# Kernel tuning notes

Measured on AMD Instinct MI355X. Metric: run time of the kernel, lower is better.

## Reference

```python
import jax, jax.numpy as jnp
import numpy as np
from math import comb

N_INPUT, N_HIDDEN, N_LATENT = 2, 1024, 16
T, B = 320, 192
DEG = N_LATENT // 2 - 1          # 7
NPTS = DEG + 1                   # 8 control points
LAT = N_LATENT + N_LATENT // 2   # 24

_COMB = jnp.array([comb(DEG, i) for i in range(NPTS)], dtype=jnp.float32)
_I = jnp.arange(NPTS, dtype=jnp.float32)


def setup_inputs() -> dict:
    key = jax.random.key(0)
    ks = jax.random.split(key, 24)
    H = N_HIDDEN
    w = lambda k, shape, sc: (jax.random.normal(k, shape, jnp.float32) * sc)
    return dict(
        x=jax.random.normal(ks[0], (T, B, N_INPUT), jnp.float32),
        latent_ctrlpt=jax.random.normal(ks[1], (B, N_LATENT), jnp.float32),
        latent_ratw=jax.random.uniform(ks[2], (B, N_LATENT // 2), jnp.float32, 0.1, 1.0),
        # h0/c0 projection linears (forward/backward directions)
        W_hf=w(ks[3], (H, LAT), 0.2), b_hf=jnp.zeros((H,), jnp.float32),
        W_hb=w(ks[4], (H, LAT), 0.2), b_hb=jnp.zeros((H,), jnp.float32),
        W_cf=w(ks[5], (H, LAT), 0.2), b_cf=jnp.zeros((H,), jnp.float32),
        W_cb=w(ks[6], (H, LAT), 0.2), b_cb=jnp.zeros((H,), jnp.float32),
        # bi-LSTM weights, PyTorch gate order (i, f, g, o)
        W_ih_f=w(ks[7], (4 * H, N_INPUT), 0.03), W_hh_f=w(ks[8], (4 * H, H), 0.03),
        b_ih_f=jnp.zeros((4 * H,), jnp.float32), b_hh_f=jnp.zeros((4 * H,), jnp.float32),
        W_ih_b=w(ks[9], (4 * H, N_INPUT), 0.03), W_hh_b=w(ks[10], (4 * H, H), 0.03),
        b_ih_b=jnp.zeros((4 * H,), jnp.float32), b_hh_b=jnp.zeros((4 * H,), jnp.float32),
        # t-logits head
        W_log=w(ks[11], (1, 2 * H), 0.03), b_log=jnp.zeros((1,), jnp.float32),
    )


def _lstm_dir(x_tm, h0, c0, W_ih, W_hh, b_ih, b_hh, reverse):
    # x_tm: (T, B, in). Precompute input projection once (compute-efficient).
    xs = jnp.einsum('tbi,gi->tbg', x_tm, W_ih) + b_ih + b_hh  # (T, B, 4H)

    def step(carry, xt):
        h, c = carry
        g = xt + h @ W_hh.T
        i, f, gg, o = jnp.split(g, 4, axis=-1)
        c = jax.nn.sigmoid(f) * c + jax.nn.sigmoid(i) * jnp.tanh(gg)
        h = jax.nn.sigmoid(o) * jnp.tanh(c)
        return (h, c), h

    _, hs = jax.lax.scan(step, (h0, c0), xs, reverse=reverse)
    return hs  # (T, B, H)


def reference(x, latent_ctrlpt, latent_ratw,
              W_hf, b_hf, W_hb, b_hb, W_cf, b_cf, W_cb, b_cb,
              W_ih_f, W_hh_f, b_ih_f, b_hh_f,
              W_ih_b, W_hh_b, b_ih_b, b_hh_b,
              W_log, b_log):
    latent = jnp.concatenate([latent_ctrlpt, latent_ratw], axis=1)  # (B, LAT)
    h0f = jnp.tanh(latent @ W_hf.T + b_hf)
    h0b = jnp.tanh(latent @ W_hb.T + b_hb)
    c0f = jnp.tanh(latent @ W_cf.T + b_cf)
    c0b = jnp.tanh(latent @ W_cb.T + b_cb)

    hf = _lstm_dir(x, h0f, c0f, W_ih_f, W_hh_f, b_ih_f, b_hh_f, reverse=False)
    hb = _lstm_dir(x, h0b, c0b, W_ih_b, W_hh_b, b_ih_b, b_hh_b, reverse=True)
    out = jnp.concatenate([hf, hb], axis=-1)           # (T, B, 2H)
    out = jnp.transpose(out, (1, 0, 2))                # batch_first (B, T, 2H)

    logits = (out @ W_log.T + b_log)[..., 0]           # (B, T)
    ts = jnp.cumsum(jax.nn.softmax(logits, axis=1), axis=1)  # (B, T) in (0, 1]

    P = latent_ctrlpt.reshape(-1, NPTS, 2)             # (B, NPTS, 2)
    r = latent_ratw.reshape(-1, NPTS)                  # (B, NPTS)

    # Rational Bezier curve, batched over B and T (replaces per-sample loop)
    t = ts[..., None]                                   # (B, T, 1)
    basis = _COMB * t ** _I * (1.0 - t) ** (DEG - _I)   # (B, T, NPTS)
    num = basis * r[:, None, :]
    w = num / num.sum(-1, keepdims=True)
    curves = jnp.einsum('btn,bnd->btd', w, P)           # (B, T, 2)

    # mean of squared consecutive control-point distances, averaged over batch
    d2 = ((P[:, 1:, :] - P[:, :-1, :]) ** 2).sum(-1)    # (B, NPTS-1)
    reg = d2.mean()
    return curves, reg
```

## Files before the change

### kernel.cpp

```cpp
#include <hip/hip_runtime.h>
#include <stdint.h>

#define T_STEPS 320
#define BATCH   192
#define HID     1024
#define NBLK    256

typedef unsigned short u16;
typedef __bf16 bf16x8 __attribute__((ext_vector_type(8)));
typedef float  f32x4  __attribute__((ext_vector_type(4)));
typedef unsigned int u32x4 __attribute__((ext_vector_type(4)));

#define OFF_BAR      0u
#define OFF_PART     16384u
#define MEMSET_BYTES 3948544u
#define OFF_C0       3948544u
#define OFF_H        5521408u
#define OFF_WPACK    7094272u
#define OFF_COEF     23871488u
#define WS_NEED      24002560u
#define OFF_HT       24002560u
#define PANEL_ELEMS  196608u
#define DIR_ELEMS    (321u * PANEL_ELEMS)
#define WS_NEED_BIG  (OFF_HT + 2ull * DIR_ELEMS * 2ull)

#define DMP_OFF_B    131072
#define DMP_WK_STRIDE 1632
#define DYN_LDS      157200

__device__ __forceinline__ u16 f2bf(float f) {
  unsigned u = __float_as_uint(f);
  unsigned r = (u + 0x7FFFu + ((u >> 16) & 1u)) >> 16;
  return (u16)r;
}
__device__ __forceinline__ float sigm(float x)   { return 1.f / (1.f + __expf(-x)); }
__device__ __forceinline__ float tanh_f(float x) { return 1.f - 2.f / (1.f + __expf(2.f * x)); }

__global__ void pack_k(const float* __restrict__ Whhf, const float* __restrict__ Whhb,
                       u16* __restrict__ wpack)
{
  int lin = blockIdx.x * 256 + threadIdx.x;
  int lane = lin & 63;
  int cg   = (lin >> 6) & 3;
  int ks   = (lin >> 8) & 31;
  int jsl  = (lin >> 13) & 63;
  int dir  = (lin >> 19) & 1;
  int col  = cg * 16 + (lane & 15);
  int R    = (col & 3) * 1024 + jsl * 16 + (col >> 2);
  int kb   = ks * 32 + (lane >> 4) * 8;
  const float* W = dir ? Whhb : Whhf;
  const float* src = W + (size_t)R * 1024 + kb;
  unsigned w[4];
  #pragma unroll
  for (int e = 0; e < 4; ++e) {
    unsigned lo = f2bf(src[2 * e]);
    unsigned hi = f2bf(src[2 * e + 1]);
    w[e] = lo | (hi << 16);
  }
  *((uint4*)(wpack + (size_t)lin * 8)) = make_uint4(w[0], w[1], w[2], w[3]);
}

__global__ void coef_k(const float* __restrict__ Wihf, const float* __restrict__ bihf,
                       const float* __restrict__ bhhf,
                       const float* __restrict__ Wihb, const float* __restrict__ bihb,
                       const float* __restrict__ bhhb, float* __restrict__ coef)
{
  int id  = blockIdx.x * 256 + threadIdx.x;
  int col = id & 63;
  int jsl = (id >> 6) & 63;
  int dir = (id >> 12) & 1;
  int R   = (col & 3) * 1024 + jsl * 16 + (col >> 2);
  const float* Wih = dir ? Wihb : Wihf;
  const float* bi  = dir ? bihb : bihf;
  const float* bh  = dir ? bhhb : bhhf;
  float4 v;
  v.x = Wih[(size_t)R * 2 + 0];
  v.y = Wih[(size_t)R * 2 + 1];
  v.z = bi[R] + bh[R];
  v.w = 0.f;
  ((float4*)coef)[id] = v;
}

__global__ void init_k(const float* __restrict__ ctrl, const float* __restrict__ ratw,
                       const float* __restrict__ Whf, const float* __restrict__ bhf,
                       const float* __restrict__ Whb, const float* __restrict__ bhb,
                       const float* __restrict__ Wcf, const float* __restrict__ bcf,
                       const float* __restrict__ Wcb, const float* __restrict__ bcb,
                       u16* hb, float* c0, size_t hstride)
{
  int idx = blockIdx.x * 256 + threadIdx.x;
  int m = blockIdx.y;
  int b = idx >> 10;
  int h = idx & 1023;
  const float* W  = (m == 0) ? Whf : (m == 1) ? Whb : (m == 2) ? Wcf : Wcb;
  const float* bi = (m == 0) ? bhf : (m == 1) ? bhb : (m == 2) ? bcf : bcb;
  float acc = bi[h];
  const float* wr = W + h * 24;
  #pragma unroll
  for (int k = 0; k < 16; ++k) acc += wr[k] * ctrl[b * 16 + k];
  #pragma unroll
  for (int k = 0; k < 8; ++k)  acc += wr[16 + k] * ratw[b * 8 + k];
  acc = tanh_f(acc);
  if (m < 2) hb[(size_t)m * hstride + (size_t)b * HID + h] = f2bf(acc);
  else       c0[((size_t)(m - 2) * BATCH + b) * HID + h] = acc;
}


#define ALD_B(S, OB) \
  asm volatile("global_load_dwordx4 %0, %1, off offset:" #OB " sc0 sc1" : "=v"(aq[S][0]) : "v"(ab0)); \
  asm volatile("global_load_dwordx4 %0, %1, off offset:" #OB " sc0 sc1" : "=v"(aq[S][1]) : "v"(ab1)); \
  asm volatile("global_load_dwordx4 %0, %1, off offset:" #OB " sc0 sc1" : "=v"(aq[S][2]) : "v"(ab2));

#define ALD_C(S, OB) \
  asm volatile("global_load_dwordx4 %0, %1, off offset:" #OB : "=v"(aq[S][0]) : "v"(ab0)); \
  asm volatile("global_load_dwordx4 %0, %1, off offset:" #OB : "=v"(aq[S][1]) : "v"(ab1)); \
  asm volatile("global_load_dwordx4 %0, %1, off offset:" #OB : "=v"(aq[S][2]) : "v"(ab2));

#define BLDS(P, C) { \
  bv[P][0] = *(const bf16x8*)(bWl + (C) * 2048 + 0);   \
  bv[P][1] = *(const bf16x8*)(bWl + (C) * 2048 + 512); \
  bv[P][2] = *(const bf16x8*)(bWl + (C) * 2048 + 1024);\
  bv[P][3] = *(const bf16x8*)(bWl + (C) * 2048 + 1536); }

#define WB(n) \
  asm volatile("s_waitcnt vmcnt(" #n ")" ::: "memory"); \
  __builtin_amdgcn_sched_barrier(0);

#define MM(C, P) { \
  _Pragma("unroll") \
  for (int mt_ = 0; mt_ < 3; ++mt_) { \
    bf16x8 a_ = __builtin_bit_cast(bf16x8, aq[C][mt_]); \
    _Pragma("unroll") \
    for (int n_ = 0; n_ < 4; ++n_) { \
      acc[mt_][n_] = __builtin_amdgcn_mfma_f32_16x16x32_bf16(a_, bv[P][n_], acc[mt_][n_], 0, 0, 0); \
    } \
  } }

#define HST(PT, VL) asm volatile("global_store_short %0, %1, off sc0 sc1" :: "v"(PT), "v"(VL) : "memory")

template<int HIST>
__launch_bounds__(512, 1)
__global__ void lstm_persist(const float* __restrict__ x,
                             const float* __restrict__ wlog,
                             float* part,
                             const float* __restrict__ c0,
                             u16* hb,
                             const u16* __restrict__ wpack,
                             const float* __restrict__ coef,
                             unsigned* bar)
{
  extern __shared__ char lds[];
  u16*   Wlds = (u16*)lds;
  float* DMP  = (float*)(lds + DMP_OFF_B);
  int*   ldsflag = (int*)(lds + DMP_OFF_B + 26112);

  const int tid   = threadIdx.x;
  const int bid   = blockIdx.x;
  const int dir   = bid >> 7;
  const int bhalf = (bid >> 6) & 1;
  const int jsl   = bid & 63;
  const int wave  = tid >> 6;
  const int lane  = tid & 63;
  const int wm    = wave >> 2;
  const int wk    = wave & 3;
  const int grp   = dir * 2 + bhalf;
  const int q4    = (lane >> 4) * 4;
  const int cl    = lane & 15;

  if (tid == 0) *ldsflag = 0;

  {
    const uint4* wsrc = (const uint4*)wpack + (size_t)(dir * 64 + jsl) * 8192;
    uint4* wdst = (uint4*)Wlds;
    #pragma unroll
    for (int i = 0; i < 16; ++i) wdst[tid + i * 512] = wsrc[tid + i * 512];
  }

  const int j    = tid & 15;
  const int rloc = tid >> 4;
  const bool pw  = (tid < 384);
  const int jglob = jsl * 16 + j;
  float4 cf0, cf1, cf2, cf3;
  {
    const float4* cp = (const float4*)coef + ((dir * 64 + jsl) * 64 + j * 4);
    cf0 = cp[0]; cf1 = cp[1]; cf2 = cp[2]; cf3 = cp[3];
  }
  const float wlg = wlog[dir * 1024 + jglob];

  float creg[4];
  int   bgm[4];
  #pragma unroll
  for (int p = 0; p < 4; ++p) {
    int bg = bhalf * 96 + p * 24 + rloc;
    bgm[p]  = bg;
    creg[p] = pw ? c0[((size_t)dir * BATCH + bg) * HID + jglob] : 0.f;
  }

  const int arow0 = bhalf * 96 + wm * 48 + 0 * 16 + cl;
  const int arow1 = arow0 + 16;
  const int arow2 = arow0 + 32;
  const int koff  = wk * 256 + (lane >> 4) * 8;
  const u16* bWl  = Wlds + (size_t)wk * 16384 + lane * 8;

  float* pbase = part + ((size_t)(dir * 8 + (jsl & 7)) * BATCH) * T_STEPS;

  unsigned* gflags = bar + grp * 1024;
  unsigned* myflag = gflags + jsl * 16;
  const unsigned* pollp = gflags + lane * 16;

  float lpv[4];
  int   lpo[4];

  __syncthreads();

  for (int s = 0; s < T_STEPS; ++s) {
    const u16* hsrc;
    u16*       hdst;
    if constexpr (HIST) {
      hsrc = hb + (size_t)dir * DIR_ELEMS + (size_t)s * PANEL_ELEMS;
      hdst = hb + (size_t)dir * DIR_ELEMS + (size_t)(s + 1) * PANEL_ELEMS;
    } else {
      const int rbuf = s & 1;
      hsrc = hb + (size_t)(dir * 2 + rbuf) * BATCH * HID;
      hdst = hb + (size_t)(dir * 2 + (rbuf ^ 1)) * BATCH * HID;
    }
    const u16* ab0 = hsrc + (size_t)arow0 * HID + koff;
    const u16* ab1 = hsrc + (size_t)arow1 * HID + koff;
    const u16* ab2 = hsrc + (size_t)arow2 * HID + koff;

    f32x4 acc[3][4];
    #pragma unroll
    for (int mt = 0; mt < 3; ++mt)
      #pragma unroll
      for (int n = 0; n < 4; ++n)
        acc[mt][n] = (f32x4){0.f, 0.f, 0.f, 0.f};

    u32x4  aq[8][3];
    bf16x8 bv[2][4];

    if constexpr (HIST) {
      ALD_C(0, 0)   ALD_C(1, 64)  ALD_C(2, 128) ALD_C(3, 192)
      ALD_C(4, 256) ALD_C(5, 320) ALD_C(6, 384) ALD_C(7, 448)
    } else {
      ALD_B(0, 0)   ALD_B(1, 64)  ALD_B(2, 128) ALD_B(3, 192)
      ALD_B(4, 256) ALD_B(5, 320) ALD_B(6, 384) ALD_B(7, 448)
    }

    BLDS(0, 0)
    BLDS(1, 1) WB(21) MM(0, 0)
    BLDS(0, 2) WB(18) MM(1, 1)
    BLDS(1, 3) WB(15) MM(2, 0)
    BLDS(0, 4) WB(12) MM(3, 1)
    BLDS(1, 5) WB(9)  MM(4, 0)
    BLDS(0, 6) WB(6)  MM(5, 1)
    BLDS(1, 7) WB(3)  MM(6, 0)
               WB(0)  MM(7, 1)

    const int t_x = dir ? (T_STEPS - 1 - s) : s;

    #pragma unroll
    for (int p = 0; p < 4; ++p) {
      if (wm == (p >> 1)) {
        const int plo = (p & 1) * 24;
        float* dst = DMP + wk * DMP_WK_STRIDE;
        #pragma unroll
        for (int mt = 0; mt < 3; ++mt)
          #pragma unroll
          for (int n = 0; n < 4; ++n)
            #pragma unroll
            for (int r = 0; r < 4; ++r) {
              int row = mt * 16 + q4 + r;
              if (row >= plo && row < plo + 24)
                dst[(row - plo) * 68 + n * 16 + cl] = acc[mt][n][r];
            }
      }
      __syncthreads();

      if (pw) {
        const int ga = rloc * 68 + (j >> 2) * 16 + (j & 3) * 4;
        f32x4 p0 = *(const f32x4*)(DMP + 0 * DMP_WK_STRIDE + ga);
        f32x4 p1 = *(const f32x4*)(DMP + 1 * DMP_WK_STRIDE + ga);
        f32x4 p2 = *(const f32x4*)(DMP + 2 * DMP_WK_STRIDE + ga);
        f32x4 p3 = *(const f32x4*)(DMP + 3 * DMP_WK_STRIDE + ga);
        f32x4 g4 = (p0 + p1) + (p2 + p3);
        int bg = bgm[p];
        float2 xv = *(const float2*)(x + ((size_t)t_x * BATCH + bg) * 2);
        float pi = g4[0] + cf0.x * xv.x + cf0.y * xv.y + cf0.z;
        float pf = g4[1] + cf1.x * xv.x + cf1.y * xv.y + cf1.z;
        float pg = g4[2] + cf2.x * xv.x + cf2.y * xv.y + cf2.z;
        float po = g4[3] + cf3.x * xv.x + cf3.y * xv.y + cf3.z;
        float ig = sigm(pi), fg = sigm(pf), gv = tanh_f(pg), og = sigm(po);
        float c = fg * creg[p] + ig * gv;
        creg[p] = c;
        float h = og * tanh_f(c);
        u16* hp = hdst + (size_t)bg * HID + jglob;
        unsigned hv = (unsigned)f2bf(h);
        HST(hp, hv);
        float lp = h * wlg;
        lp += __shfl_xor(lp, 1);
        lp += __shfl_xor(lp, 2);
        lp += __shfl_xor(lp, 4);
        lp += __shfl_xor(lp, 8);
        lpv[p] = lp;
        lpo[p] = bg * T_STEPS + t_x;
      }
      __syncthreads();
    }

    asm volatile("s_waitcnt vmcnt(0)" ::: "memory");
    __syncthreads();

    if (pw && j == 0) {
      atomicAdd(&pbase[lpo[0]], lpv[0]);
      atomicAdd(&pbase[lpo[1]], lpv[1]);
      atomicAdd(&pbase[lpo[2]], lpv[2]);
      atomicAdd(&pbase[lpo[3]], lpv[3]);
    }

    if (tid == 0) {
      unsigned nv = (unsigned)(s + 1);
      asm volatile("global_store_dword %0, %1, off sc0 sc1" :: "v"(myflag), "v"(nv) : "memory");
    }
    if (wave == 0) {
      const unsigned tgt = (unsigned)(s + 1);
      long guard = 0;
      for (;;) {
        unsigned fv;
        asm volatile("global_load_dword %0, %1, off sc0 sc1" : "=v"(fv) : "v"(pollp));
        asm volatile("s_waitcnt vmcnt(0)" ::: "memory");
        if (__all(fv >= tgt)) break;
        if (++guard > (1L << 20)) { if (lane == 0) *ldsflag = 1; break; }
        __builtin_amdgcn_s_sleep(1);
      }
    }
    __syncthreads();
    if (*ldsflag) return;
  }
}

__global__ void post_k(const float* __restrict__ part, const float* __restrict__ ctrl,
                       const float* __restrict__ ratw, float* __restrict__ out)
{
  __shared__ float sh[T_STEPS + 64];
  const int b = blockIdx.x;
  const int t = threadIdx.x;
  float l = 0.f;
  #pragma unroll
  for (int p = 0; p < 16; ++p)
    l += part[((size_t)p * BATCH + b) * T_STEPS + t];
  sh[t] = l;
  __syncthreads();
  if (t < 64) {
    float mm = sh[t];
    for (int i = t + 64; i < T_STEPS; i += 64) mm = fmaxf(mm, sh[i]);
    #pragma unroll
    for (int o = 32; o; o >>= 1) mm = fmaxf(mm, __shfl_xor(mm, o));
    if (t == 0) sh[T_STEPS] = mm;
  }
  __syncthreads();
  const float m = sh[T_STEPS];
  float e = __expf(l - m);
  __syncthreads();
  sh[t] = e;
  __syncthreads();
  for (int off = 1; off < T_STEPS; off <<= 1) {
    float v = (t >= off) ? sh[t - off] : 0.f;
    __syncthreads();
    sh[t] += v;
    __syncthreads();
  }
  const float total = sh[T_STEPS - 1];
  const float ts = sh[t] / total;

  float px[8], py[8], rr[8];
  #pragma unroll
  for (int n = 0; n < 8; ++n) {
    px[n] = ctrl[b * 16 + 2 * n];
    py[n] = ctrl[b * 16 + 2 * n + 1];
    rr[n] = ratw[b * 8 + n];
  }
  const float C[8] = {1.f, 7.f, 21.f, 35.f, 35.f, 21.f, 7.f, 1.f};
  float tp[8], up[8];
  tp[0] = 1.f; up[0] = 1.f;
  const float u = 1.f - ts;
  #pragma unroll
  for (int n = 1; n < 8; ++n) { tp[n] = tp[n - 1] * ts; up[n] = up[n - 1] * u; }
  float den = 0.f, nx = 0.f, ny = 0.f;
  #pragma unroll
  for (int n = 0; n < 8; ++n) {
    float w = C[n] * tp[n] * up[7 - n] * rr[n];
    den += w; nx += w * px[n]; ny += w * py[n];
  }
  out[(b * T_STEPS + t) * 2 + 0] = nx / den;
  out[(b * T_STEPS + t) * 2 + 1] = ny / den;

  if (b == 0) {
    __syncthreads();
    if (t < BATCH) {
      float s2 = 0.f;
      #pragma unroll
      for (int n = 0; n < 7; ++n) {
        float dx = ctrl[t * 16 + 2 * n + 2] - ctrl[t * 16 + 2 * n + 0];
        float dy = ctrl[t * 16 + 2 * n + 3] - ctrl[t * 16 + 2 * n + 1];
        s2 += dx * dx + dy * dy;
      }
      sh[t] = s2;
    }
    __syncthreads();
    if (t == 0) {
      float tot = 0.f;
      for (int i = 0; i < BATCH; ++i) tot += sh[i];
      out[BATCH * T_STEPS * 2] = tot / (float)(BATCH * 7);
    }
  }
}

extern "C" void kernel_launch(void* const* d_in, const int* in_sizes, int n_in,
                              void* d_out, int out_size, void* d_ws, size_t ws_size,
                              hipStream_t stream)
{
  const float* x    = (const float*)d_in[0];
  const float* ctrl = (const float*)d_in[1];
  const float* ratw = (const float*)d_in[2];
  const float* Whf  = (const float*)d_in[3];
  const float* bhf  = (const float*)d_in[4];
  const float* Whb  = (const float*)d_in[5];
  const float* bhb  = (const float*)d_in[6];
  const float* Wcf  = (const float*)d_in[7];
  const float* bcf  = (const float*)d_in[8];
  const float* Wcb  = (const float*)d_in[9];
  const float* bcb  = (const float*)d_in[10];
  const float* Wihf = (const float*)d_in[11];
  const float* Whhf = (const float*)d_in[12];
  const float* bihf = (const float*)d_in[13];
  const float* bhhf = (const float*)d_in[14];
  const float* Wihb = (const float*)d_in[15];
  const float* Whhb = (const float*)d_in[16];
  const float* bihb = (const float*)d_in[17];
  const float* bhhb = (const float*)d_in[18];
  const float* Wlog = (const float*)d_in[19];
  float* out = (float*)d_out;
  char*  ws  = (char*)d_ws;
  if (ws_size < (size_t)WS_NEED) return;

  const bool big = (ws_size >= (size_t)WS_NEED_BIG);

  unsigned* bar    = (unsigned*)(ws + OFF_BAR);
  float*    part   = (float*)(ws + OFF_PART);
  float*    c0     = (float*)(ws + OFF_C0);
  u16*      hsmall = (u16*)(ws + OFF_H);
  u16*      hbig   = (u16*)(ws + OFF_HT);
  u16*      wpack  = (u16*)(ws + OFF_WPACK);
  float*    coef   = (float*)(ws + OFF_COEF);

  u16*   hb      = big ? hbig : hsmall;
  size_t hstride = big ? (size_t)DIR_ELEMS : (size_t)2 * BATCH * HID;

  hipMemsetAsync(ws, 0, MEMSET_BYTES, stream);
  pack_k<<<4096, 256, 0, stream>>>(Whhf, Whhb, wpack);
  coef_k<<<32, 256, 0, stream>>>(Wihf, bihf, bhhf, Wihb, bihb, bhhb, coef);
  init_k<<<dim3(768, 4), 256, 0, stream>>>(ctrl, ratw, Whf, bhf, Whb, bhb,
                                           Wcf, bcf, Wcb, bcb, hb, c0, hstride);
  if (big) {
    hipFuncSetAttribute((const void*)lstm_persist<1>,
                        hipFuncAttributeMaxDynamicSharedMemorySize, DYN_LDS);
    lstm_persist<1><<<NBLK, 512, DYN_LDS, stream>>>(x, Wlog, part, c0, hb, wpack, coef, bar);
  } else {
    hipFuncSetAttribute((const void*)lstm_persist<0>,
                        hipFuncAttributeMaxDynamicSharedMemorySize, DYN_LDS);
    lstm_persist<0><<<NBLK, 512, DYN_LDS, stream>>>(x, Wlog, part, c0, hb, wpack, coef, bar);
  }
  post_k<<<BATCH, T_STEPS, 0, stream>>>(part, ctrl, ratw, out);
}
```

Baseline: 3.717 ms.

## Use ring of hidden-state panels with periodic cache invalidation

Replaces the full per-timestep hidden-state history (which needed a very large workspace) with a ring of P panels sized from the available workspace. The cached-load path, which reads h without cache bypass, now stays correct by issuing buffer_inv every P-2 steps, before any panel is reused. This lets the cached path run with smaller workspaces, at the cost of occasional invalidations and an extra block barrier. It also moves the step-completion flag store ahead of the logit atomics so other blocks are released sooner.

```diff
diff --git a/kernel.cpp b/kernel.cpp
--- a/kernel.cpp
+++ b/kernel.cpp
@@ -21,8 +21,8 @@
 #define WS_NEED      24002560u
 #define OFF_HT       24002560u
 #define PANEL_ELEMS  196608u
-#define DIR_ELEMS    (321u * PANEL_ELEMS)
-#define WS_NEED_BIG  (OFF_HT + 2ull * DIR_ELEMS * 2ull)
+#define PANEL_BYTES  393216u
+#define P_COST       786432u
 
 #define DMP_OFF_B    131072
 #define DMP_WK_STRIDE 1632
@@ -116,29 +116,29 @@
   asm volatile("global_load_dwordx4 %0, %1, off offset:" #OB : "=v"(aq[S][1]) : "v"(ab1)); \
   asm volatile("global_load_dwordx4 %0, %1, off offset:" #OB : "=v"(aq[S][2]) : "v"(ab2));
 
-#define BLDS(P, C) { \
-  bv[P][0] = *(const bf16x8*)(bWl + (C) * 2048 + 0);   \
-  bv[P][1] = *(const bf16x8*)(bWl + (C) * 2048 + 512); \
-  bv[P][2] = *(const bf16x8*)(bWl + (C) * 2048 + 1024);\
-  bv[P][3] = *(const bf16x8*)(bWl + (C) * 2048 + 1536); }
+#define BLDS(P_, C) { \
+  bv[P_][0] = *(const bf16x8*)(bWl + (C) * 2048 + 0);   \
+  bv[P_][1] = *(const bf16x8*)(bWl + (C) * 2048 + 512); \
+  bv[P_][2] = *(const bf16x8*)(bWl + (C) * 2048 + 1024);\
+  bv[P_][3] = *(const bf16x8*)(bWl + (C) * 2048 + 1536); }
 
 #define WB(n) \
   asm volatile("s_waitcnt vmcnt(" #n ")" ::: "memory"); \
   __builtin_amdgcn_sched_barrier(0);
 
-#define MM(C, P) { \
+#define MM(C, P_) { \
   _Pragma("unroll") \
   for (int mt_ = 0; mt_ < 3; ++mt_) { \
     bf16x8 a_ = __builtin_bit_cast(bf16x8, aq[C][mt_]); \
     _Pragma("unroll") \
     for (int n_ = 0; n_ < 4; ++n_) { \
-      acc[mt_][n_] = __builtin_amdgcn_mfma_f32_16x16x32_bf16(a_, bv[P][n_], acc[mt_][n_], 0, 0, 0); \
+      acc[mt_][n_] = __builtin_amdgcn_mfma_f32_16x16x32_bf16(a_, bv[P_][n_], acc[mt_][n_], 0, 0, 0); \
     } \
   } }
 
 #define HST(PT, VL) asm volatile("global_store_short %0, %1, off sc0 sc1" :: "v"(PT), "v"(VL) : "memory")
 
-template<int HIST>
+template<int CACHED>
 __launch_bounds__(512, 1)
 __global__ void lstm_persist(const float* __restrict__ x,
                              const float* __restrict__ wlog,
@@ -147,7 +147,8 @@
                              u16* hb,
                              const u16* __restrict__ wpack,
                              const float* __restrict__ coef,
-                             unsigned* bar)
+                             unsigned* bar,
+                             int PN, int IV)
 {
   extern __shared__ char lds[];
   u16*   Wlds = (u16*)lds;
@@ -211,19 +212,27 @@
   float lpv[4];
   int   lpo[4];
 
+  int sp   = 0;
+  int invc = 0;
+
   __syncthreads();
 
   for (int s = 0; s < T_STEPS; ++s) {
-    const u16* hsrc;
-    u16*       hdst;
-    if constexpr (HIST) {
-      hsrc = hb + (size_t)dir * DIR_ELEMS + (size_t)s * PANEL_ELEMS;
-      hdst = hb + (size_t)dir * DIR_ELEMS + (size_t)(s + 1) * PANEL_ELEMS;
-    } else {
-      const int rbuf = s & 1;
-      hsrc = hb + (size_t)(dir * 2 + rbuf) * BATCH * HID;
-      hdst = hb + (size_t)(dir * 2 + (rbuf ^ 1)) * BATCH * HID;
-    }
+    if constexpr (CACHED) {
+      if (invc == 0) {
+        if (wave == 0) {
+          asm volatile("buffer_inv sc0 sc1" ::: "memory");
+          asm volatile("s_waitcnt vmcnt(0)" ::: "memory");
+        }
+        __syncthreads();
+      }
+      if (++invc >= IV) invc = 0;
+    }
+
+    int dp = sp + 1; if (dp == PN) dp = 0;
+    const u16* hsrc = hb + ((size_t)(dir * PN + sp)) * PANEL_ELEMS;
+    u16*       hdst = hb + ((size_t)(dir * PN + dp)) * PANEL_ELEMS;
+    sp = dp;
     const u16* ab0 = hsrc + (size_t)arow0 * HID + koff;
     const u16* ab1 = hsrc + (size_t)arow1 * HID + koff;
     const u16* ab2 = hsrc + (size_t)arow2 * HID + koff;
@@ -238,7 +247,7 @@
     u32x4  aq[8][3];
     bf16x8 bv[2][4];
 
-    if constexpr (HIST) {
+    if constexpr (CACHED) {
       ALD_C(0, 0)   ALD_C(1, 64)  ALD_C(2, 128) ALD_C(3, 192)
       ALD_C(4, 256) ALD_C(5, 320) ALD_C(6, 384) ALD_C(7, 448)
     } else {
@@ -310,16 +319,15 @@
     asm volatile("s_waitcnt vmcnt(0)" ::: "memory");
     __syncthreads();
 
+    if (tid == 0) {
+      unsigned nv = (unsigned)(s + 1);
+      asm volatile("global_store_dword %0, %1, off sc0 sc1" :: "v"(myflag), "v"(nv) : "memory");
+    }
     if (pw && j == 0) {
       atomicAdd(&pbase[lpo[0]], lpv[0]);
       atomicAdd(&pbase[lpo[1]], lpv[1]);
       atomicAdd(&pbase[lpo[2]], lpv[2]);
       atomicAdd(&pbase[lpo[3]], lpv[3]);
-    }
-
-    if (tid == 0) {
-      unsigned nv = (unsigned)(s + 1);
-      asm volatile("global_store_dword %0, %1, off sc0 sc1" :: "v"(myflag), "v"(nv) : "memory");
     }
     if (wave == 0) {
       const unsigned tgt = (unsigned)(s + 1);
@@ -443,32 +451,37 @@
   char*  ws  = (char*)d_ws;
   if (ws_size < (size_t)WS_NEED) return;
 
-  const bool big = (ws_size >= (size_t)WS_NEED_BIG);
+  size_t availB = (ws_size > (size_t)OFF_HT) ? (ws_size - (size_t)OFF_HT) : 0;
+  long Pl = (long)(availB / (size_t)P_COST);
+  int P = (int)(Pl > 322 ? 322 : Pl);
+  const bool cached = (P >= 18);
 
   unsigned* bar    = (unsigned*)(ws + OFF_BAR);
   float*    part   = (float*)(ws + OFF_PART);
   float*    c0     = (float*)(ws + OFF_C0);
   u16*      hsmall = (u16*)(ws + OFF_H);
-  u16*      hbig   = (u16*)(ws + OFF_HT);
+  u16*      hring  = (u16*)(ws + OFF_HT);
   u16*      wpack  = (u16*)(ws + OFF_WPACK);
   float*    coef   = (float*)(ws + OFF_COEF);
 
-  u16*   hb      = big ? hbig : hsmall;
-  size_t hstride = big ? (size_t)DIR_ELEMS : (size_t)2 * BATCH * HID;
+  u16*   hb      = cached ? hring : hsmall;
+  int    PN      = cached ? P : 2;
+  int    IV      = (cached && P < 322) ? (P - 2) : (1 << 30);
+  size_t hstride = (size_t)PN * PANEL_ELEMS;
 
   hipMemsetAsync(ws, 0, MEMSET_BYTES, stream);
   pack_k<<<4096, 256, 0, stream>>>(Whhf, Whhb, wpack);
   coef_k<<<32, 256, 0, stream>>>(Wihf, bihf, bhhf, Wihb, bihb, bhhb, coef);
   init_k<<<dim3(768, 4), 256, 0, stream>>>(ctrl, ratw, Whf, bhf, Whb, bhb,
                                            Wcf, bcf, Wcb, bcb, hb, c0, hstride);
-  if (big) {
+  if (cached) {
     hipFuncSetAttribute((const void*)lstm_persist<1>,
                         hipFuncAttributeMaxDynamicSharedMemorySize, DYN_LDS);
-    lstm_persist<1><<<NBLK, 512, DYN_LDS, stream>>>(x, Wlog, part, c0, hb, wpack, coef, bar);
+    lstm_persist<1><<<NBLK, 512, DYN_LDS, stream>>>(x, Wlog, part, c0, hb, wpack, coef, bar, PN, IV);
   } else {
     hipFuncSetAttribute((const void*)lstm_persist<0>,
                         hipFuncAttributeMaxDynamicSharedMemorySize, DYN_LDS);
-    lstm_persist<0><<<NBLK, 512, DYN_LDS, stream>>>(x, Wlog, part, c0, hb, wpack, coef, bar);
+    lstm_persist<0><<<NBLK, 512, DYN_LDS, stream>>>(x, Wlog, part, c0, hb, wpack, coef, bar, PN, IV);
   }
   post_k<<<BATCH, T_STEPS, 0, stream>>>(part, ctrl, ratw, out);
 }
```

New measurement: 3.680 ms. About the same (-1.0%).
